# Performance work log

Hardware: AMD Instinct MI355X
Metric: run time of the kernel (lower is better)

The kernel has to match this reference:

```python
import jax, jax.numpy as jnp
import numpy as np

NUM_HEADS = 8
NEG_INF = -1e9

def setup_inputs() -> dict:
    key = jax.random.key(0)
    k1, k2 = jax.random.split(key)
    B, S, D = 2, 4096, 512
    inputs = jax.random.normal(k1, (B, S, D), dtype=jnp.float32)
    # glorot-style scale for the fused QKV weight
    qkv_weights = jax.random.normal(k2, (D, 3 * D), dtype=jnp.float32) * (1.0 / np.sqrt(D))
    return {"inputs": inputs, "qkv_weights": qkv_weights}

def reference(inputs, qkv_weights):
    B, S, D = inputs.shape
    H = NUM_HEADS
    d = D // H  # head dim
    qkv = jnp.einsum('bsd,de->bse', inputs, qkv_weights)  # (B,S,3D)
    q, k, v = jnp.split(qkv, 3, axis=-1)
    # (B,S,D) -> (B,H,S,d)
    def split_heads(x):
        return x.reshape(B, S, H, d).transpose(0, 2, 1, 3)
    q, k, v = split_heads(q), split_heads(k), split_heads(v)
    scores = jnp.einsum('bhid,bhjd->bhij', q, k) / jnp.sqrt(jnp.asarray(d, inputs.dtype))
    # causal mask as in source: tril * scores + (-1e9) * upper-triangle
    tril = jnp.tril(jnp.ones((S, S), dtype=inputs.dtype))
    scores = tril * scores + NEG_INF * (1.0 - tril)
    a = jax.nn.softmax(scores, axis=-1)
    out = jnp.einsum('bhij,bhjd->bhid', a, v)  # (B,H,S,d)
    return out.transpose(0, 2, 1, 3).reshape(B, S, D)
```

## Files before the change

kernel.cpp:

```cpp
#include <hip/hip_runtime.h>

typedef unsigned short u16;
typedef __bf16 b16;
typedef b16 b16x8 __attribute__((ext_vector_type(8)));
typedef float f32x4 __attribute__((ext_vector_type(4)));
typedef u16 u16x4 __attribute__((ext_vector_type(4)));
typedef u16 u16x8 __attribute__((ext_vector_type(8)));
typedef float f4 __attribute__((ext_vector_type(4)));

#define NH 8
#define SEQ 4096
#define DM 512
#define HDIM 64
#define GM 8192
#define GK 512
#define GN 1536

#define QSCALE 0.18033688011112042f
#define SMBIAS 14.0f

__device__ __forceinline__ u16 f2bf(float f) {
  b16 h = (b16)f;
  return __builtin_bit_cast(u16, h);
}

__device__ __forceinline__ void gl16(const u16* g, u16* l) {
  __builtin_amdgcn_global_load_lds((const __attribute__((address_space(1))) void*)g,
                                   (__attribute__((address_space(3))) void*)l, 16, 0, 0);
}

__global__ __launch_bounds__(256) void cvt_fused(const float* __restrict__ x,
                                                 u16* __restrict__ y,
                                                 const float* __restrict__ w,
                                                 u16* __restrict__ wt) {
  __shared__ float tile[32][33];
  int bid = blockIdx.x;
  int t = threadIdx.x;
  if (bid < 2048) {
    int i = (bid * 256 + t) * 8;
    f4 a = *(const f4*)(x + i);
    f4 b = *(const f4*)(x + i + 4);
    u16x8 o;
    o[0] = f2bf(a[0]); o[1] = f2bf(a[1]); o[2] = f2bf(a[2]); o[3] = f2bf(a[3]);
    o[4] = f2bf(b[0]); o[5] = f2bf(b[1]); o[6] = f2bf(b[2]); o[7] = f2bf(b[3]);
    *(u16x8*)(y + i) = o;
  } else {
    int q = bid - 2048;
    int n0 = (q % 48) * 32;
    int k0 = (q / 48) * 32;
    int tn = t & 31, tk = t >> 5;
#pragma unroll
    for (int p = 0; p < 4; ++p) {
      int k = tk + p * 8;
      tile[k][tn] = w[(k0 + k) * GN + n0 + tn];
    }
    __syncthreads();
    int n_l = t >> 3, kg = (t & 7) * 4;
    u16x4 o;
#pragma unroll
    for (int i2 = 0; i2 < 4; ++i2) o[i2] = f2bf(tile[kg + i2][n_l]);
    *(u16x4*)(wt + (n0 + n_l) * GK + k0 + kg) = o;
  }
}

__global__ __launch_bounds__(256, 3) void qkv_gemm(const u16* __restrict__ A,
                                                   const u16* __restrict__ Wt,
                                                   u16* __restrict__ Q,
                                                   u16* __restrict__ K,
                                                   u16* __restrict__ V) {
  __shared__ __align__(16) u16 As[3][4096];
  __shared__ __align__(16) u16 Bs[3][4096];
  int bm = blockIdx.x * 128;
  int bn = blockIdx.y * 128;
  int t = threadIdx.x;
  int lane = t & 63, w = t >> 6;
  int wr = w >> 1, wc = w & 1;
  int l15 = lane & 15, g = lane >> 4;

  f32x4 acc[4][4];
#pragma unroll
  for (int i = 0; i < 4; ++i)
#pragma unroll
    for (int j = 0; j < 4; ++j) {
      acc[i][j][0] = 0.f; acc[i][j][1] = 0.f; acc[i][j][2] = 0.f; acc[i][j][3] = 0.f;
    }

#define GSTAGE(slot, k0) do {                                                   \
    _Pragma("unroll")                                                           \
    for (int p = 0; p < 2; ++p) {                                               \
      int cid = p * 256 + t;                                                    \
      int row = cid >> 2, co = (cid & 3) * 8;                                   \
      gl16(A + (size_t)(bm + row) * GK + (k0) + co, &As[slot][cid * 8]);        \
      gl16(Wt + (size_t)(bn + row) * GK + (k0) + co, &Bs[slot][cid * 8]);       \
    }                                                                           \
  } while (0)

  GSTAGE(0, 0);
  GSTAGE(1, 32);
  int cur = 0;
  for (int kk = 0; kk < 16; ++kk) {
    asm volatile("s_waitcnt vmcnt(4)" ::: "memory");
    __builtin_amdgcn_s_barrier();
    int pk = kk + 2 < 16 ? kk + 2 : 15;
    int slot = cur + 2; if (slot >= 3) slot -= 3;
    GSTAGE(slot, pk * 32);

    b16x8 af[4], bf[4];
#pragma unroll
    for (int mi = 0; mi < 4; ++mi)
      af[mi] = *(const b16x8*)(&As[cur][(wr * 64 + mi * 16 + l15) * 32 + g * 8]);
#pragma unroll
    for (int ni = 0; ni < 4; ++ni)
      bf[ni] = *(const b16x8*)(&Bs[cur][(wc * 64 + ni * 16 + l15) * 32 + g * 8]);
    __builtin_amdgcn_s_setprio(1);
#pragma unroll
    for (int mi = 0; mi < 4; ++mi)
#pragma unroll
      for (int ni = 0; ni < 4; ++ni)
        acc[mi][ni] = __builtin_amdgcn_mfma_f32_16x16x32_bf16(af[mi], bf[ni], acc[mi][ni], 0, 0, 0);
    __builtin_amdgcn_s_setprio(0);
    cur = (cur == 2) ? 0 : cur + 1;
  }

#pragma unroll
  for (int mi = 0; mi < 4; ++mi)
#pragma unroll
    for (int ni = 0; ni < 4; ++ni) {
      int e = bn + wc * 64 + ni * 16 + l15;
      int which = e >> 9, col = e & 511;
      int h = col >> 6, dd = col & 63;
      u16* dst = which == 0 ? Q : (which == 1 ? K : V);
      float scale = (which == 0) ? QSCALE : 1.0f;
#pragma unroll
      for (int r = 0; r < 4; ++r) {
        int m = bm + wr * 64 + mi * 16 + g * 4 + r;
        int b = m >> 12, s = m & 4095;
        dst[(((b * NH + h) * SEQ) + s) * HDIM + dd] = f2bf(acc[mi][ni][r] * scale);
      }
    }
}

__global__ __launch_bounds__(256) void transpose_v(const u16* __restrict__ V,
                                                   u16* __restrict__ Vt) {
  __shared__ u16 tl[64][72];
  int bh = blockIdx.x >> 6;
  int s0 = (blockIdx.x & 63) * 64;
  const u16* src = V + ((size_t)bh * SEQ + s0) * HDIM;
  u16* dst = Vt + (size_t)bh * HDIM * SEQ + s0;
  int t = threadIdx.x;
#pragma unroll
  for (int p = 0; p < 2; ++p) {
    int cid = p * 256 + t;
    int row = cid >> 3, ch = cid & 7;
    *(u16x8*)(&tl[row][ch * 8]) = *(const u16x8*)(src + row * HDIM + ch * 8);
  }
  __syncthreads();
#pragma unroll
  for (int p = 0; p < 4; ++p) {
    int cid = p * 256 + t;
    int dd = cid >> 4, l = cid & 15;
    u16x4 o;
#pragma unroll
    for (int c = 0; c < 4; ++c) o[c] = tl[c * 16 + l][dd];
    *(u16x4*)(dst + dd * SEQ + l * 4) = o;
  }
}

__global__ __launch_bounds__(256, 4) void attn(const u16* __restrict__ Q,
                                               const u16* __restrict__ Kv,
                                               const u16* __restrict__ Vtg,
                                               float* __restrict__ out) {
  int id = blockIdx.x;
  int bh = id & 15;
  int i = id >> 4;
  int j = i & 15, pp = i >> 4;
  int qt = (pp == 0) ? 63 - j : (pp == 1) ? j : (pp == 2) ? 47 - j : 16 + j;
  int b = bh >> 3, h = bh & 7;
  const u16* Qb = Q + (size_t)bh * SEQ * HDIM;
  const u16* Kb = Kv + (size_t)bh * SEQ * HDIM;
  const u16* Vb = Vtg + (size_t)bh * HDIM * SEQ;
  int t = threadIdx.x, lane = t & 63, w = t >> 6;
  int l15 = lane & 15, g = lane >> 4;
  int qb = qt * 64;
  int qw = qb + w * 16;

  __shared__ __align__(16) u16 Ks[2][4096];
  __shared__ __align__(16) u16 Vs[2][4096];
  __shared__ __align__(16) u16 Ps[4096];

  int rsub = lane >> 3, cp = lane & 7;
  int ch = cp ^ rsub;
  int xorp = (l15 & 7) << 3;

  b16x8 qf[2];
#pragma unroll
  for (int ks = 0; ks < 2; ++ks)
    qf[ks] = *(const b16x8*)(Qb + (qw + l15) * HDIM + ks * 32 + g * 8);

  b16x8 vone;
#pragma unroll
  for (int ii = 0; ii < 8; ++ii) vone[ii] = __builtin_bit_cast(b16, (u16)0x3F80);

  f32x4 oacc[4], lacc;
#pragma unroll
  for (int ii = 0; ii < 4; ++ii) {
    oacc[ii][0] = 0.f; oacc[ii][1] = 0.f; oacc[ii][2] = 0.f; oacc[ii][3] = 0.f;
    lacc[ii] = 0.f;
  }

#define STAGE(slot, jj) do {                                                    \
    _Pragma("unroll")                                                           \
    for (int p = 0; p < 2; ++p) {                                               \
      int row = (w * 2 + p) * 8 + rsub;                                         \
      gl16(Kb + (size_t)((jj) + row) * HDIM + ch * 8, &Ks[slot][(w * 2 + p) * 512]); \
      gl16(Vb + (size_t)row * SEQ + (jj) + ch * 8, &Vs[slot][(w * 2 + p) * 512]);    \
    }                                                                           \
  } while (0)

#define QKT(sx, slot) do {                                                      \
    _Pragma("unroll")                                                           \
    for (int c = 0; c < 4; ++c) {                                               \
      sx[c][0] = -SMBIAS; sx[c][1] = -SMBIAS; sx[c][2] = -SMBIAS; sx[c][3] = -SMBIAS; \
    }                                                                           \
    _Pragma("unroll")                                                           \
    for (int c = 0; c < 4; ++c) {                                               \
      const u16* kr = Ks[slot] + (c * 16 + l15) * 64;                           \
      b16x8 kf0 = *(const b16x8*)(kr + ((g * 8) ^ xorp));                       \
      b16x8 kf1 = *(const b16x8*)(kr + ((32 + g * 8) ^ xorp));                  \
      sx[c] = __builtin_amdgcn_mfma_f32_16x16x32_bf16(qf[0], kf0, sx[c], 0, 0, 0); \
      sx[c] = __builtin_amdgcn_mfma_f32_16x16x32_bf16(qf[1], kf1, sx[c], 0, 0, 0); \
    }                                                                           \
  } while (0)

#define SMSTORE(sx, jj) do {                                                    \
    if ((jj) + 63 > qw) {                                                       \
      _Pragma("unroll")                                                         \
      for (int c = 0; c < 4; ++c)                                               \
        _Pragma("unroll")                                                       \
        for (int r = 0; r < 4; ++r) {                                           \
          int col = (jj) + c * 16 + l15;                                        \
          int qq = qw + g * 4 + r;                                              \
          if (col > qq) sx[c][r] = -1e30f;                                      \
        }                                                                       \
    }                                                                           \
    _Pragma("unroll")                                                           \
    for (int r = 0; r < 4; ++r) {                                               \
      u16x4 pw;                                                                 \
      _Pragma("unroll")                                                         \
      for (int c = 0; c < 4; ++c)                                               \
        pw[c] = f2bf(__builtin_amdgcn_exp2f(sx[c][r]));                         \
      int prow = w * 16 + g * 4 + r;                                            \
      *(u16x4*)(Ps + prow * 64 + ((l15 * 4) ^ ((prow & 7) << 3))) = pw;         \
    }                                                                           \
  } while (0)

  int nt = qt + 1;

  STAGE(0, 0);
  asm volatile("s_waitcnt vmcnt(0)" ::: "memory");
  __builtin_amdgcn_s_barrier();
  if (nt > 1) STAGE(1, 64);
  {
    f32x4 s0[4];
    QKT(s0, 0);
    SMSTORE(s0, 0);
  }

  int cur = 0;
  for (int tt = 0; tt < nt; ++tt) {
    asm volatile("s_waitcnt vmcnt(0)" ::: "memory");
    __builtin_amdgcn_s_barrier();

    b16x8 vfr[2][4];
#pragma unroll
    for (int js = 0; js < 2; ++js)
#pragma unroll
      for (int tdd = 0; tdd < 4; ++tdd)
        vfr[js][tdd] = *(const b16x8*)(Vs[cur] + (tdd * 16 + l15) * 64 + ((js * 32 + g * 8) ^ xorp));
    asm volatile("s_waitcnt lgkmcnt(0)" ::: "memory");
    __builtin_amdgcn_s_barrier();

    if (tt + 2 < nt) STAGE(cur, (tt + 2) * 64);

    bool more = (tt + 1 < nt);
    f32x4 sb[4];
    __builtin_amdgcn_s_setprio(1);
    if (more) QKT(sb, cur ^ 1);

#pragma unroll
    for (int js = 0; js < 2; ++js) {
      int eoff = (js * 32 + g * 8) ^ xorp;
      b16x8 pf = *(const b16x8*)(Ps + (w * 16 + l15) * 64 + eoff);
      lacc = __builtin_amdgcn_mfma_f32_16x16x32_bf16(pf, vone, lacc, 0, 0, 0);
#pragma unroll
      for (int tdd = 0; tdd < 4; ++tdd)
        oacc[tdd] = __builtin_amdgcn_mfma_f32_16x16x32_bf16(pf, vfr[js][tdd], oacc[tdd], 0, 0, 0);
    }
    __builtin_amdgcn_s_setprio(0);

    if (more) SMSTORE(sb, (tt + 1) * 64);
    cur ^= 1;
  }

  float inv[4];
#pragma unroll
  for (int r = 0; r < 4; ++r) inv[r] = 1.0f / lacc[r];
#pragma unroll
  for (int tdd = 0; tdd < 4; ++tdd)
#pragma unroll
    for (int r = 0; r < 4; ++r) {
      int q = qw + g * 4 + r;
      int dd = tdd * 16 + l15;
      out[((size_t)b * SEQ + q) * DM + h * HDIM + dd] = oacc[tdd][r] * inv[r];
    }
}

extern "C" void kernel_launch(void* const* d_in, const int* in_sizes, int n_in,
                              void* d_out, int out_size, void* d_ws, size_t ws_size,
                              hipStream_t stream) {
  const float* x = (const float*)d_in[0];
  const float* wq = (const float*)d_in[1];
  float* out = (float*)d_out;
  char* ws = (char*)d_ws;

  u16* A  = (u16*)ws;
  u16* Wt = (u16*)(ws + 8388608);
  u16* Qw = (u16*)(ws + 8388608 + 1572864);
  u16* Kw = Qw + 4194304;
  u16* Vw = Kw + 4194304;
  u16* Vt = A;

  cvt_fused<<<2816, 256, 0, stream>>>(x, A, wq, Wt);
  dim3 gg(64, 12);
  qkv_gemm<<<gg, 256, 0, stream>>>(A, Wt, Qw, Kw, Vw);
  transpose_v<<<1024, 256, 0, stream>>>(Vw, Vt);
  attn<<<1024, 256, 0, stream>>>(Qw, Kw, Vt, out);
}
```

Before: 92.49 us.

## Double query tile per attention block to reuse K/V tiles across two row groups

Each attention block now handles 128 query rows instead of 64: every wave computes two 16-row subtiles that share the same staged K and V fragments, and the grid is halved to 512 blocks with a simpler causal ordering. The aim is to halve K/V global and LDS traffic per output row and raise MFMA density per LDS read. The cost is more registers (launch bounds lowered to 3 waves per SIMD), a larger P buffer, fewer blocks for load balancing, and extra masked work on the diagonal tiles.

```diff
diff --git a/kernel.cpp b/kernel.cpp
--- a/kernel.cpp
+++ b/kernel.cpp
@@ -166,46 +166,50 @@
   }
 }
 
-__global__ __launch_bounds__(256, 4) void attn(const u16* __restrict__ Q,
+__global__ __launch_bounds__(256, 3) void attn(const u16* __restrict__ Q,
                                                const u16* __restrict__ Kv,
                                                const u16* __restrict__ Vtg,
                                                float* __restrict__ out) {
   int id = blockIdx.x;
   int bh = id & 15;
   int i = id >> 4;
-  int j = i & 15, pp = i >> 4;
-  int qt = (pp == 0) ? 63 - j : (pp == 1) ? j : (pp == 2) ? 47 - j : 16 + j;
+  int qt = (i < 16) ? 31 - i : i - 16;
   int b = bh >> 3, h = bh & 7;
   const u16* Qb = Q + (size_t)bh * SEQ * HDIM;
   const u16* Kb = Kv + (size_t)bh * SEQ * HDIM;
   const u16* Vb = Vtg + (size_t)bh * HDIM * SEQ;
   int t = threadIdx.x, lane = t & 63, w = t >> 6;
   int l15 = lane & 15, g = lane >> 4;
-  int qb = qt * 64;
-  int qw = qb + w * 16;
+  int qb = qt * 128;
+  int qw = qb + w * 32;
 
   __shared__ __align__(16) u16 Ks[2][4096];
   __shared__ __align__(16) u16 Vs[2][4096];
-  __shared__ __align__(16) u16 Ps[4096];
+  __shared__ __align__(16) u16 Ps[8192];
 
   int rsub = lane >> 3, cp = lane & 7;
   int ch = cp ^ rsub;
   int xorp = (l15 & 7) << 3;
 
-  b16x8 qf[2];
-#pragma unroll
-  for (int ks = 0; ks < 2; ++ks)
-    qf[ks] = *(const b16x8*)(Qb + (qw + l15) * HDIM + ks * 32 + g * 8);
+  b16x8 qf[2][2];
+#pragma unroll
+  for (int sub = 0; sub < 2; ++sub)
+#pragma unroll
+    for (int ks = 0; ks < 2; ++ks)
+      qf[sub][ks] = *(const b16x8*)(Qb + (qw + sub * 16 + l15) * HDIM + ks * 32 + g * 8);
 
   b16x8 vone;
 #pragma unroll
   for (int ii = 0; ii < 8; ++ii) vone[ii] = __builtin_bit_cast(b16, (u16)0x3F80);
 
-  f32x4 oacc[4], lacc;
-#pragma unroll
-  for (int ii = 0; ii < 4; ++ii) {
-    oacc[ii][0] = 0.f; oacc[ii][1] = 0.f; oacc[ii][2] = 0.f; oacc[ii][3] = 0.f;
-    lacc[ii] = 0.f;
+  f32x4 oacc[2][4], lacc[2];
+#pragma unroll
+  for (int sub = 0; sub < 2; ++sub) {
+#pragma unroll
+    for (int ii = 0; ii < 4; ++ii) {
+      oacc[sub][ii][0] = 0.f; oacc[sub][ii][1] = 0.f; oacc[sub][ii][2] = 0.f; oacc[sub][ii][3] = 0.f;
+    }
+    lacc[sub][0] = 0.f; lacc[sub][1] = 0.f; lacc[sub][2] = 0.f; lacc[sub][3] = 0.f;
   }
 
 #define STAGE(slot, jj) do {                                                    \
@@ -217,53 +221,62 @@
     }                                                                           \
   } while (0)
 
-#define QKT(sx, slot) do {                                                      \
-    _Pragma("unroll")                                                           \
-    for (int c = 0; c < 4; ++c) {                                               \
-      sx[c][0] = -SMBIAS; sx[c][1] = -SMBIAS; sx[c][2] = -SMBIAS; sx[c][3] = -SMBIAS; \
-    }                                                                           \
+#define QKT2(sx, slot) do {                                                     \
+    _Pragma("unroll")                                                           \
+    for (int sub = 0; sub < 2; ++sub)                                           \
+      _Pragma("unroll")                                                         \
+      for (int c = 0; c < 4; ++c) {                                             \
+        sx[sub][c][0] = -SMBIAS; sx[sub][c][1] = -SMBIAS;                       \
+        sx[sub][c][2] = -SMBIAS; sx[sub][c][3] = -SMBIAS;                       \
+      }                                                                         \
     _Pragma("unroll")                                                           \
     for (int c = 0; c < 4; ++c) {                                               \
       const u16* kr = Ks[slot] + (c * 16 + l15) * 64;                           \
       b16x8 kf0 = *(const b16x8*)(kr + ((g * 8) ^ xorp));                       \
       b16x8 kf1 = *(const b16x8*)(kr + ((32 + g * 8) ^ xorp));                  \
-      sx[c] = __builtin_amdgcn_mfma_f32_16x16x32_bf16(qf[0], kf0, sx[c], 0, 0, 0); \
-      sx[c] = __builtin_amdgcn_mfma_f32_16x16x32_bf16(qf[1], kf1, sx[c], 0, 0, 0); \
+      sx[0][c] = __builtin_amdgcn_mfma_f32_16x16x32_bf16(qf[0][0], kf0, sx[0][c], 0, 0, 0); \
+      sx[1][c] = __builtin_amdgcn_mfma_f32_16x16x32_bf16(qf[1][0], kf0, sx[1][c], 0, 0, 0); \
+      sx[0][c] = __builtin_amdgcn_mfma_f32_16x16x32_bf16(qf[0][1], kf1, sx[0][c], 0, 0, 0); \
+      sx[1][c] = __builtin_amdgcn_mfma_f32_16x16x32_bf16(qf[1][1], kf1, sx[1][c], 0, 0, 0); \
     }                                                                           \
   } while (0)
 
-#define SMSTORE(sx, jj) do {                                                    \
-    if ((jj) + 63 > qw) {                                                       \
+#define SMSTORE2(sx, jj) do {                                                   \
+    _Pragma("unroll")                                                           \
+    for (int sub = 0; sub < 2; ++sub) {                                         \
+      int qsub = qw + sub * 16;                                                 \
+      if ((jj) + 63 > qsub) {                                                   \
+        _Pragma("unroll")                                                       \
+        for (int c = 0; c < 4; ++c)                                             \
+          _Pragma("unroll")                                                     \
+          for (int r = 0; r < 4; ++r) {                                         \
+            int col = (jj) + c * 16 + l15;                                      \
+            int qq = qsub + g * 4 + r;                                          \
+            if (col > qq) sx[sub][c][r] = -1e30f;                               \
+          }                                                                     \
+      }                                                                         \
       _Pragma("unroll")                                                         \
-      for (int c = 0; c < 4; ++c)                                               \
+      for (int r = 0; r < 4; ++r) {                                             \
+        u16x4 pw;                                                               \
         _Pragma("unroll")                                                       \
-        for (int r = 0; r < 4; ++r) {                                           \
-          int col = (jj) + c * 16 + l15;                                        \
-          int qq = qw + g * 4 + r;                                              \
-          if (col > qq) sx[c][r] = -1e30f;                                      \
-        }                                                                       \
-    }                                                                           \
-    _Pragma("unroll")                                                           \
-    for (int r = 0; r < 4; ++r) {                                               \
-      u16x4 pw;                                                                 \
-      _Pragma("unroll")                                                         \
-      for (int c = 0; c < 4; ++c)                                               \
-        pw[c] = f2bf(__builtin_amdgcn_exp2f(sx[c][r]));                         \
-      int prow = w * 16 + g * 4 + r;                                            \
-      *(u16x4*)(Ps + prow * 64 + ((l15 * 4) ^ ((prow & 7) << 3))) = pw;         \
+        for (int c = 0; c < 4; ++c)                                             \
+          pw[c] = f2bf(__builtin_amdgcn_exp2f(sx[sub][c][r]));                  \
+        int prow = w * 32 + sub * 16 + g * 4 + r;                               \
+        *(u16x4*)(Ps + prow * 64 + ((l15 * 4) ^ ((prow & 7) << 3))) = pw;       \
+      }                                                                         \
     }                                                                           \
   } while (0)
 
-  int nt = qt + 1;
+  int nt = 2 * qt + 2;
 
   STAGE(0, 0);
   asm volatile("s_waitcnt vmcnt(0)" ::: "memory");
   __builtin_amdgcn_s_barrier();
-  if (nt > 1) STAGE(1, 64);
+  STAGE(1, 64);
   {
-    f32x4 s0[4];
-    QKT(s0, 0);
-    SMSTORE(s0, 0);
+    f32x4 s0[2][4];
+    QKT2(s0, 0);
+    SMSTORE2(s0, 0);
   }
 
   int cur = 0;
@@ -283,36 +296,43 @@
     if (tt + 2 < nt) STAGE(cur, (tt + 2) * 64);
 
     bool more = (tt + 1 < nt);
-    f32x4 sb[4];
+    f32x4 sb[2][4];
     __builtin_amdgcn_s_setprio(1);
-    if (more) QKT(sb, cur ^ 1);
+    if (more) QKT2(sb, cur ^ 1);
 
 #pragma unroll
     for (int js = 0; js < 2; ++js) {
       int eoff = (js * 32 + g * 8) ^ xorp;
-      b16x8 pf = *(const b16x8*)(Ps + (w * 16 + l15) * 64 + eoff);
-      lacc = __builtin_amdgcn_mfma_f32_16x16x32_bf16(pf, vone, lacc, 0, 0, 0);
-#pragma unroll
-      for (int tdd = 0; tdd < 4; ++tdd)
-        oacc[tdd] = __builtin_amdgcn_mfma_f32_16x16x32_bf16(pf, vfr[js][tdd], oacc[tdd], 0, 0, 0);
+      b16x8 pf0 = *(const b16x8*)(Ps + (w * 32 + l15) * 64 + eoff);
+      b16x8 pf1 = *(const b16x8*)(Ps + (w * 32 + 16 + l15) * 64 + eoff);
+      lacc[0] = __builtin_amdgcn_mfma_f32_16x16x32_bf16(pf0, vone, lacc[0], 0, 0, 0);
+      lacc[1] = __builtin_amdgcn_mfma_f32_16x16x32_bf16(pf1, vone, lacc[1], 0, 0, 0);
+#pragma unroll
+      for (int tdd = 0; tdd < 4; ++tdd) {
+        oacc[0][tdd] = __builtin_amdgcn_mfma_f32_16x16x32_bf16(pf0, vfr[js][tdd], oacc[0][tdd], 0, 0, 0);
+        oacc[1][tdd] = __builtin_amdgcn_mfma_f32_16x16x32_bf16(pf1, vfr[js][tdd], oacc[1][tdd], 0, 0, 0);
+      }
     }
     __builtin_amdgcn_s_setprio(0);
 
-    if (more) SMSTORE(sb, (tt + 1) * 64);
+    if (more) SMSTORE2(sb, (tt + 1) * 64);
     cur ^= 1;
   }
 
-  float inv[4];
-#pragma unroll
-  for (int r = 0; r < 4; ++r) inv[r] = 1.0f / lacc[r];
-#pragma unroll
-  for (int tdd = 0; tdd < 4; ++tdd)
-#pragma unroll
-    for (int r = 0; r < 4; ++r) {
-      int q = qw + g * 4 + r;
-      int dd = tdd * 16 + l15;
-      out[((size_t)b * SEQ + q) * DM + h * HDIM + dd] = oacc[tdd][r] * inv[r];
-    }
+#pragma unroll
+  for (int sub = 0; sub < 2; ++sub) {
+    float inv[4];
+#pragma unroll
+    for (int r = 0; r < 4; ++r) inv[r] = 1.0f / lacc[sub][r];
+#pragma unroll
+    for (int tdd = 0; tdd < 4; ++tdd)
+#pragma unroll
+      for (int r = 0; r < 4; ++r) {
+        int q = qw + sub * 16 + g * 4 + r;
+        int dd = tdd * 16 + l15;
+        out[((size_t)b * SEQ + q) * DM + h * HDIM + dd] = oacc[sub][tdd][r] * inv[r];
+      }
+  }
 }
 
 extern "C" void kernel_launch(void* const* d_in, const int* in_sizes, int n_in,
@@ -334,5 +354,5 @@
   dim3 gg(64, 12);
   qkv_gemm<<<gg, 256, 0, stream>>>(A, Wt, Qw, Kw, Vw);
   transpose_v<<<1024, 256, 0, stream>>>(Vw, Vt);
-  attn<<<1024, 256, 0, stream>>>(Qw, Kw, Vt, out);
-}
+  attn<<<512, 256, 0, stream>>>(Qw, Kw, Vt, out);
+}
```

New measurement: 116.4 us. 25.8% more time.

## Compute transposed scores so P stays in registers, drop P shared buffer

Applied to the files above, without the earlier changes.

The attention kernel now computes S^T (K as the A operand, Q as B), so the exponentiated probabilities land in registers already laid out as the B operand of the PV MFMA, and the P round trip through shared memory disappears. V gets a triple-buffered LDS ring, and V fragments are read inline, which removes the per-iteration V register preload and its extra barrier. To match the operand layout, the V transpose kernel permutes key columns within each 64-block. This cuts LDS traffic and one barrier per tile, at the cost of a more intricate index permutation that has to agree with the MFMA register layout.

```diff
diff --git a/kernel.cpp b/kernel.cpp
--- a/kernel.cpp
+++ b/kernel.cpp
@@ -158,11 +158,13 @@
 #pragma unroll
   for (int p = 0; p < 4; ++p) {
     int cid = p * 256 + t;
-    int dd = cid >> 4, l = cid & 15;
+    int dd = cid >> 4, idx = cid & 15;
+    int c = idx >> 2, g = idx & 3;
+    int base = (c >> 1) * 32 + g * 8 + (c & 1) * 4;
     u16x4 o;
 #pragma unroll
-    for (int c = 0; c < 4; ++c) o[c] = tl[c * 16 + l][dd];
-    *(u16x4*)(dst + dd * SEQ + l * 4) = o;
+    for (int r = 0; r < 4; ++r) o[r] = tl[c * 16 + g * 4 + r][dd];
+    *(u16x4*)(dst + dd * SEQ + base) = o;
   }
 }
 
@@ -185,8 +187,7 @@
   int qw = qb + w * 16;
 
   __shared__ __align__(16) u16 Ks[2][4096];
-  __shared__ __align__(16) u16 Vs[2][4096];
-  __shared__ __align__(16) u16 Ps[4096];
+  __shared__ __align__(16) u16 Vs[3][4096];
 
   int rsub = lane >> 3, cp = lane & 7;
   int ch = cp ^ rsub;
@@ -201,118 +202,102 @@
 #pragma unroll
   for (int ii = 0; ii < 8; ++ii) vone[ii] = __builtin_bit_cast(b16, (u16)0x3F80);
 
-  f32x4 oacc[4], lacc;
+  f32x4 oaccT[4], lacc;
 #pragma unroll
   for (int ii = 0; ii < 4; ++ii) {
-    oacc[ii][0] = 0.f; oacc[ii][1] = 0.f; oacc[ii][2] = 0.f; oacc[ii][3] = 0.f;
+    oaccT[ii][0] = 0.f; oaccT[ii][1] = 0.f; oaccT[ii][2] = 0.f; oaccT[ii][3] = 0.f;
     lacc[ii] = 0.f;
   }
-
-#define STAGE(slot, jj) do {                                                    \
+  b16x8 ptp[2];
+
+#define STAGE2(kslot, vslot, jj) do {                                           \
     _Pragma("unroll")                                                           \
     for (int p = 0; p < 2; ++p) {                                               \
       int row = (w * 2 + p) * 8 + rsub;                                         \
-      gl16(Kb + (size_t)((jj) + row) * HDIM + ch * 8, &Ks[slot][(w * 2 + p) * 512]); \
-      gl16(Vb + (size_t)row * SEQ + (jj) + ch * 8, &Vs[slot][(w * 2 + p) * 512]);    \
+      gl16(Kb + (size_t)((jj) + row) * HDIM + ch * 8, &Ks[kslot][(w * 2 + p) * 512]); \
+      gl16(Vb + (size_t)row * SEQ + (jj) + ch * 8, &Vs[vslot][(w * 2 + p) * 512]);   \
     }                                                                           \
   } while (0)
 
-#define QKT(sx, slot) do {                                                      \
+#define QKT(st, kslot) do {                                                     \
     _Pragma("unroll")                                                           \
     for (int c = 0; c < 4; ++c) {                                               \
-      sx[c][0] = -SMBIAS; sx[c][1] = -SMBIAS; sx[c][2] = -SMBIAS; sx[c][3] = -SMBIAS; \
+      st[c][0] = -SMBIAS; st[c][1] = -SMBIAS; st[c][2] = -SMBIAS; st[c][3] = -SMBIAS; \
     }                                                                           \
     _Pragma("unroll")                                                           \
     for (int c = 0; c < 4; ++c) {                                               \
-      const u16* kr = Ks[slot] + (c * 16 + l15) * 64;                           \
+      const u16* kr = Ks[kslot] + (c * 16 + l15) * 64;                          \
       b16x8 kf0 = *(const b16x8*)(kr + ((g * 8) ^ xorp));                       \
       b16x8 kf1 = *(const b16x8*)(kr + ((32 + g * 8) ^ xorp));                  \
-      sx[c] = __builtin_amdgcn_mfma_f32_16x16x32_bf16(qf[0], kf0, sx[c], 0, 0, 0); \
-      sx[c] = __builtin_amdgcn_mfma_f32_16x16x32_bf16(qf[1], kf1, sx[c], 0, 0, 0); \
+      st[c] = __builtin_amdgcn_mfma_f32_16x16x32_bf16(kf0, qf[0], st[c], 0, 0, 0); \
+      st[c] = __builtin_amdgcn_mfma_f32_16x16x32_bf16(kf1, qf[1], st[c], 0, 0, 0); \
     }                                                                           \
   } while (0)
 
-#define SMSTORE(sx, jj) do {                                                    \
+#define SMREG(st, jj, ptX) do {                                                 \
     if ((jj) + 63 > qw) {                                                       \
+      int qq = qw + l15;                                                        \
       _Pragma("unroll")                                                         \
       for (int c = 0; c < 4; ++c)                                               \
         _Pragma("unroll")                                                       \
         for (int r = 0; r < 4; ++r) {                                           \
-          int col = (jj) + c * 16 + l15;                                        \
-          int qq = qw + g * 4 + r;                                              \
-          if (col > qq) sx[c][r] = -1e30f;                                      \
+          int kvg = (jj) + c * 16 + g * 4 + r;                                  \
+          if (kvg > qq) st[c][r] = -1e30f;                                      \
         }                                                                       \
     }                                                                           \
     _Pragma("unroll")                                                           \
-    for (int r = 0; r < 4; ++r) {                                               \
-      u16x4 pw;                                                                 \
+    for (int c = 0; c < 4; ++c)                                                 \
       _Pragma("unroll")                                                         \
-      for (int c = 0; c < 4; ++c)                                               \
-        pw[c] = f2bf(__builtin_amdgcn_exp2f(sx[c][r]));                         \
-      int prow = w * 16 + g * 4 + r;                                            \
-      *(u16x4*)(Ps + prow * 64 + ((l15 * 4) ^ ((prow & 7) << 3))) = pw;         \
-    }                                                                           \
+      for (int r = 0; r < 4; ++r)                                               \
+        ptX[c >> 1][(c & 1) * 4 + r] = (b16)__builtin_amdgcn_exp2f(st[c][r]);   \
   } while (0)
 
   int nt = qt + 1;
 
-  STAGE(0, 0);
+  STAGE2(0, 0, 0);
   asm volatile("s_waitcnt vmcnt(0)" ::: "memory");
   __builtin_amdgcn_s_barrier();
-  if (nt > 1) STAGE(1, 64);
+  if (nt > 1) STAGE2(1, 1, 64);
   {
     f32x4 s0[4];
     QKT(s0, 0);
-    SMSTORE(s0, 0);
-  }
-
-  int cur = 0;
+    SMREG(s0, 0, ptp);
+  }
+
   for (int tt = 0; tt < nt; ++tt) {
     asm volatile("s_waitcnt vmcnt(0)" ::: "memory");
     __builtin_amdgcn_s_barrier();
 
-    b16x8 vfr[2][4];
-#pragma unroll
-    for (int js = 0; js < 2; ++js)
-#pragma unroll
-      for (int tdd = 0; tdd < 4; ++tdd)
-        vfr[js][tdd] = *(const b16x8*)(Vs[cur] + (tdd * 16 + l15) * 64 + ((js * 32 + g * 8) ^ xorp));
-    asm volatile("s_waitcnt lgkmcnt(0)" ::: "memory");
-    __builtin_amdgcn_s_barrier();
-
-    if (tt + 2 < nt) STAGE(cur, (tt + 2) * 64);
+    if (tt + 2 < nt) STAGE2(tt & 1, (tt + 2) % 3, (tt + 2) * 64);
 
     bool more = (tt + 1 < nt);
-    f32x4 sb[4];
+    f32x4 st[4];
     __builtin_amdgcn_s_setprio(1);
-    if (more) QKT(sb, cur ^ 1);
-
-#pragma unroll
-    for (int js = 0; js < 2; ++js) {
-      int eoff = (js * 32 + g * 8) ^ xorp;
-      b16x8 pf = *(const b16x8*)(Ps + (w * 16 + l15) * 64 + eoff);
-      lacc = __builtin_amdgcn_mfma_f32_16x16x32_bf16(pf, vone, lacc, 0, 0, 0);
-#pragma unroll
-      for (int tdd = 0; tdd < 4; ++tdd)
-        oacc[tdd] = __builtin_amdgcn_mfma_f32_16x16x32_bf16(pf, vfr[js][tdd], oacc[tdd], 0, 0, 0);
+    if (more) QKT(st, (tt + 1) & 1);
+
+    const u16* Vc = Vs[tt % 3];
+#pragma unroll
+    for (int ks = 0; ks < 2; ++ks) {
+      int eoff = (ks * 32 + g * 8);
+      lacc = __builtin_amdgcn_mfma_f32_16x16x32_bf16(vone, ptp[ks], lacc, 0, 0, 0);
+#pragma unroll
+      for (int tdd = 0; tdd < 4; ++tdd) {
+        b16x8 vf = *(const b16x8*)(Vc + (tdd * 16 + l15) * 64 + (eoff ^ xorp));
+        oaccT[tdd] = __builtin_amdgcn_mfma_f32_16x16x32_bf16(vf, ptp[ks], oaccT[tdd], 0, 0, 0);
+      }
     }
     __builtin_amdgcn_s_setprio(0);
 
-    if (more) SMSTORE(sb, (tt + 1) * 64);
-    cur ^= 1;
-  }
-
-  float inv[4];
-#pragma unroll
-  for (int r = 0; r < 4; ++r) inv[r] = 1.0f / lacc[r];
+    if (more) SMREG(st, (tt + 1) * 64, ptp);
+  }
+
+  float inv = 1.0f / lacc[0];
+  size_t rowbase = ((size_t)b * SEQ + qw + l15) * DM + h * HDIM;
 #pragma unroll
   for (int tdd = 0; tdd < 4; ++tdd)
 #pragma unroll
-    for (int r = 0; r < 4; ++r) {
-      int q = qw + g * 4 + r;
-      int dd = tdd * 16 + l15;
-      out[((size_t)b * SEQ + q) * DM + h * HDIM + dd] = oacc[tdd][r] * inv[r];
-    }
+    for (int r = 0; r < 4; ++r)
+      out[rowbase + tdd * 16 + g * 4 + r] = oaccT[tdd][r] * inv;
 }
 
 extern "C" void kernel_launch(void* const* d_in, const int* in_sizes, int n_in,
```

Result: faster. 88.89 us (-3.9%).
